# Optimization experiments

Hardware: AMD Instinct MI355X
Metric: run time of the kernel (lower is better)

The kernel has to match this reference:

```python
import jax, jax.numpy as jnp
import numpy as np

OOV_INDEX = -1
VOCAB = 50257
HID = 1024

def setup_inputs() -> dict:
    key = jax.random.key(0)
    ks = jax.random.split(key, 7)
    scale = 1.0 / np.sqrt(HID)
    inp = {
        "input": jax.random.randint(ks[0], (1,), 0, VOCAB, dtype=jnp.int64)
                 if jax.config.jax_enable_x64 else
                 jax.random.randint(ks[0], (1,), 0, VOCAB, dtype=jnp.int32),
        "hidden": jax.random.normal(ks[1], (1, 1, HID), dtype=jnp.float32),
        "emb": jax.random.normal(ks[2], (VOCAB, HID), dtype=jnp.float32),
        # PyTorch GRU packs gates as [reset; update; new] along dim 0
        "w_ih": jax.random.uniform(ks[3], (3 * HID, HID), jnp.float32, -scale, scale),
        "w_hh": jax.random.uniform(ks[4], (3 * HID, HID), jnp.float32, -scale, scale),
        "b_ih": jax.random.uniform(ks[5], (3 * HID,), jnp.float32, -scale, scale),
        "b_hh": jax.random.uniform(ks[6], (3 * HID,), jnp.float32, -scale, scale),
    }
    return inp

def reference(input, hidden, emb, w_ih, w_hh, b_ih, b_hh):
    # Embedding lookup with OOV (-1) -> zero vector, matching the torch branch.
    idx = jnp.maximum(input[0], 0)
    looked = emb[idx]                                   # [H]
    x = jnp.where(input[0] == OOV_INDEX, jnp.zeros_like(looked), looked)  # [H]
    h = hidden[0, 0]                                    # [H]
    # Single GRU step (PyTorch gate ordering: r, z, n)
    gi = w_ih @ x + b_ih                                # [3H]
    gh = w_hh @ h + b_hh                                # [3H]
    i_r, i_z, i_n = jnp.split(gi, 3)
    h_r, h_z, h_n = jnp.split(gh, 3)
    r = jax.nn.sigmoid(i_r + h_r)
    z = jax.nn.sigmoid(i_z + h_z)
    n = jnp.tanh(i_n + r * h_n)
    h_new = (1.0 - z) * n + z * h                       # [H]
    out = h_new.reshape(1, 1, HID)
    return (out, out)
```

## Files before the change

kernel.cpp:

```cpp
#include <hip/hip_runtime.h>

#define HID 1024

__global__ __launch_bounds__(256) void gru_step_kernel(
    const int*   __restrict__ inp,
    const float* __restrict__ hidden,
    const float* __restrict__ emb,
    const float* __restrict__ w_ih,
    const float* __restrict__ w_hh,
    const float* __restrict__ b_ih,
    const float* __restrict__ b_hh,
    float*       __restrict__ out)
{
    const int lane = threadIdx.x & 63;
    const int j    = (blockIdx.x * blockDim.x + threadIdx.x) >> 6;
    if (j >= HID) return;

    const int   token = inp[0];
    const int   idx   = token < 0 ? 0 : token;
    const float xmask = (token == -1) ? 0.0f : 1.0f;

    const float* __restrict__ xrow = emb + (size_t)idx * HID;

    const float* __restrict__ r0 = w_ih + (size_t)j * HID;
    const float* __restrict__ r1 = r0 + (size_t)HID * HID;
    const float* __restrict__ r2 = r1 + (size_t)HID * HID;
    const float* __restrict__ r3 = w_hh + (size_t)j * HID;
    const float* __restrict__ r4 = r3 + (size_t)HID * HID;
    const float* __restrict__ r5 = r4 + (size_t)HID * HID;

    float a0 = 0.f, a1 = 0.f, a2 = 0.f, a3 = 0.f, a4 = 0.f, a5 = 0.f;

    #pragma unroll
    for (int k = 0; k < 4; ++k) {
        const int off = k * 256 + lane * 4;
        const float4 xv = *(const float4*)(xrow   + off);
        const float4 hv = *(const float4*)(hidden + off);
        float4 w;
        w = *(const float4*)(r0 + off);
        a0 += w.x * xv.x + w.y * xv.y + w.z * xv.z + w.w * xv.w;
        w = *(const float4*)(r1 + off);
        a1 += w.x * xv.x + w.y * xv.y + w.z * xv.z + w.w * xv.w;
        w = *(const float4*)(r2 + off);
        a2 += w.x * xv.x + w.y * xv.y + w.z * xv.z + w.w * xv.w;
        w = *(const float4*)(r3 + off);
        a3 += w.x * hv.x + w.y * hv.y + w.z * hv.z + w.w * hv.w;
        w = *(const float4*)(r4 + off);
        a4 += w.x * hv.x + w.y * hv.y + w.z * hv.z + w.w * hv.w;
        w = *(const float4*)(r5 + off);
        a5 += w.x * hv.x + w.y * hv.y + w.z * hv.z + w.w * hv.w;
    }

    #pragma unroll
    for (int s = 32; s > 0; s >>= 1) {
        a0 += __shfl_xor(a0, s);
        a1 += __shfl_xor(a1, s);
        a2 += __shfl_xor(a2, s);
        a3 += __shfl_xor(a3, s);
        a4 += __shfl_xor(a4, s);
        a5 += __shfl_xor(a5, s);
    }

    if (lane == 0) {
        const float i_r = xmask * a0 + b_ih[j];
        const float i_z = xmask * a1 + b_ih[j + HID];
        const float i_n = xmask * a2 + b_ih[j + 2 * HID];
        const float h_r = a3 + b_hh[j];
        const float h_z = a4 + b_hh[j + HID];
        const float h_n = a5 + b_hh[j + 2 * HID];

        const float r = 1.0f / (1.0f + expf(-(i_r + h_r)));
        const float z = 1.0f / (1.0f + expf(-(i_z + h_z)));
        const float n = tanhf(i_n + r * h_n);
        const float h = hidden[j];
        const float hn = (1.0f - z) * n + z * h;

        out[j]       = hn;
        out[j + HID] = hn;
    }
}

extern "C" void kernel_launch(void* const* d_in, const int* in_sizes, int n_in,
                              void* d_out, int out_size, void* d_ws, size_t ws_size,
                              hipStream_t stream) {
    const int*   inp    = (const int*)  d_in[0];
    const float* hidden = (const float*)d_in[1];
    const float* emb    = (const float*)d_in[2];
    const float* w_ih   = (const float*)d_in[3];
    const float* w_hh   = (const float*)d_in[4];
    const float* b_ih   = (const float*)d_in[5];
    const float* b_hh   = (const float*)d_in[6];
    float* out = (float*)d_out;

    gru_step_kernel<<<dim3(256), dim3(256), 0, stream>>>(
        inp, hidden, emb, w_ih, w_hh, b_ih, b_hh, out);
}
```

Baseline: 9.685 us.

## Assign one block per output row and reduce across waves via shared memory

Changes the work split so each of 1024 blocks handles one hidden unit, with all 256 threads each loading one float4 from each of the six weight rows, instead of one wave per row looping four times. Partial dot products are reduced within each wave by shuffles, then across the four waves through shared memory and a barrier. This raises the number of concurrent memory requests and the block count to better saturate bandwidth on a 24 MB weight stream, at the cost of four times more blocks, an added block barrier, and redundant x/h loads per block.

Result: no change. 9.593 us (-1.0%).

```diff
diff --git a/kernel.cpp b/kernel.cpp
--- a/kernel.cpp
+++ b/kernel.cpp
@@ -12,44 +12,41 @@
     const float* __restrict__ b_hh,
     float*       __restrict__ out)
 {
-    const int lane = threadIdx.x & 63;
-    const int j    = (blockIdx.x * blockDim.x + threadIdx.x) >> 6;
-    if (j >= HID) return;
+    __shared__ float part[4][6];
+
+    const int tid  = threadIdx.x;
+    const int lane = tid & 63;
+    const int wv   = tid >> 6;
+    const int j    = blockIdx.x;
+    const int off  = tid * 4;
 
     const int   token = inp[0];
     const int   idx   = token < 0 ? 0 : token;
     const float xmask = (token == -1) ? 0.0f : 1.0f;
 
-    const float* __restrict__ xrow = emb + (size_t)idx * HID;
+    const float4 xv = *(const float4*)(emb + (size_t)idx * HID + off);
+    const float4 hv = *(const float4*)(hidden + off);
 
-    const float* __restrict__ r0 = w_ih + (size_t)j * HID;
+    const float* __restrict__ r0 = w_ih + (size_t)j * HID + off;
     const float* __restrict__ r1 = r0 + (size_t)HID * HID;
     const float* __restrict__ r2 = r1 + (size_t)HID * HID;
-    const float* __restrict__ r3 = w_hh + (size_t)j * HID;
+    const float* __restrict__ r3 = w_hh + (size_t)j * HID + off;
     const float* __restrict__ r4 = r3 + (size_t)HID * HID;
     const float* __restrict__ r5 = r4 + (size_t)HID * HID;
 
-    float a0 = 0.f, a1 = 0.f, a2 = 0.f, a3 = 0.f, a4 = 0.f, a5 = 0.f;
+    const float4 w0 = *(const float4*)r0;
+    const float4 w1 = *(const float4*)r1;
+    const float4 w2 = *(const float4*)r2;
+    const float4 w3 = *(const float4*)r3;
+    const float4 w4 = *(const float4*)r4;
+    const float4 w5 = *(const float4*)r5;
 
-    #pragma unroll
-    for (int k = 0; k < 4; ++k) {
-        const int off = k * 256 + lane * 4;
-        const float4 xv = *(const float4*)(xrow   + off);
-        const float4 hv = *(const float4*)(hidden + off);
-        float4 w;
-        w = *(const float4*)(r0 + off);
-        a0 += w.x * xv.x + w.y * xv.y + w.z * xv.z + w.w * xv.w;
-        w = *(const float4*)(r1 + off);
-        a1 += w.x * xv.x + w.y * xv.y + w.z * xv.z + w.w * xv.w;
-        w = *(const float4*)(r2 + off);
-        a2 += w.x * xv.x + w.y * xv.y + w.z * xv.z + w.w * xv.w;
-        w = *(const float4*)(r3 + off);
-        a3 += w.x * hv.x + w.y * hv.y + w.z * hv.z + w.w * hv.w;
-        w = *(const float4*)(r4 + off);
-        a4 += w.x * hv.x + w.y * hv.y + w.z * hv.z + w.w * hv.w;
-        w = *(const float4*)(r5 + off);
-        a5 += w.x * hv.x + w.y * hv.y + w.z * hv.z + w.w * hv.w;
-    }
+    float a0 = w0.x * xv.x + w0.y * xv.y + w0.z * xv.z + w0.w * xv.w;
+    float a1 = w1.x * xv.x + w1.y * xv.y + w1.z * xv.z + w1.w * xv.w;
+    float a2 = w2.x * xv.x + w2.y * xv.y + w2.z * xv.z + w2.w * xv.w;
+    float a3 = w3.x * hv.x + w3.y * hv.y + w3.z * hv.z + w3.w * hv.w;
+    float a4 = w4.x * hv.x + w4.y * hv.y + w4.z * hv.z + w4.w * hv.w;
+    float a5 = w5.x * hv.x + w5.y * hv.y + w5.z * hv.z + w5.w * hv.w;
 
     #pragma unroll
     for (int s = 32; s > 0; s >>= 1) {
@@ -62,12 +59,25 @@
     }
 
     if (lane == 0) {
-        const float i_r = xmask * a0 + b_ih[j];
-        const float i_z = xmask * a1 + b_ih[j + HID];
-        const float i_n = xmask * a2 + b_ih[j + 2 * HID];
-        const float h_r = a3 + b_hh[j];
-        const float h_z = a4 + b_hh[j + HID];
-        const float h_n = a5 + b_hh[j + 2 * HID];
+        part[wv][0] = a0; part[wv][1] = a1; part[wv][2] = a2;
+        part[wv][3] = a3; part[wv][4] = a4; part[wv][5] = a5;
+    }
+    __syncthreads();
+
+    if (tid == 0) {
+        const float s0 = part[0][0] + part[1][0] + part[2][0] + part[3][0];
+        const float s1 = part[0][1] + part[1][1] + part[2][1] + part[3][1];
+        const float s2 = part[0][2] + part[1][2] + part[2][2] + part[3][2];
+        const float s3 = part[0][3] + part[1][3] + part[2][3] + part[3][3];
+        const float s4 = part[0][4] + part[1][4] + part[2][4] + part[3][4];
+        const float s5 = part[0][5] + part[1][5] + part[2][5] + part[3][5];
+
+        const float i_r = xmask * s0 + b_ih[j];
+        const float i_z = xmask * s1 + b_ih[j + HID];
+        const float i_n = xmask * s2 + b_ih[j + 2 * HID];
+        const float h_r = s3 + b_hh[j];
+        const float h_z = s4 + b_hh[j + HID];
+        const float h_n = s5 + b_hh[j + 2 * HID];
 
         const float r = 1.0f / (1.0f + expf(-(i_r + h_r)));
         const float z = 1.0f / (1.0f + expf(-(i_z + h_z)));
@@ -92,6 +102,6 @@
     const float* b_hh   = (const float*)d_in[6];
     float* out = (float*)d_out;
 
-    gru_step_kernel<<<dim3(256), dim3(256), 0, stream>>>(
+    gru_step_kernel<<<dim3(HID), dim3(256), 0, stream>>>(
         inp, hidden, emb, w_ih, w_hh, b_ih, b_hh, out);
 }
```
